# Kernel optimization log

Measured on AMD Instinct MI355X. Metric: run time of the kernel, lower is better.

## Reference

```python
import jax, jax.numpy as jnp
import numpy as np

N_NODES = 100000
N_EDGES = 1600000


def spmm(edge_index, edge_vals, x, n_nodes):
    # adj @ x with adj in COO form: out[dst] += val * x[src]
    src = edge_index[0]
    dst = edge_index[1]
    gathered = x[src] * edge_vals[:, None]  # [E, F]
    return jax.ops.segment_sum(gathered, dst, num_segments=n_nodes)


def setup_inputs() -> dict:
    key = jax.random.key(0)
    ks = jax.random.split(key, 8)
    x = jax.random.normal(ks[0], (N_NODES, 512), dtype=jnp.float32)
    edge_index = jax.random.randint(ks[1], (2, N_EDGES), 0, N_NODES, dtype=jnp.int64)
    edge_vals = jax.random.uniform(ks[2], (N_EDGES,), dtype=jnp.float32)
    # xavier-uniform style weights, zero biases (as in initialize_weights)
    def xavier(k, fan_in, fan_out):
        lim = float(np.sqrt(6.0 / (fan_in + fan_out)))
        return jax.random.uniform(k, (fan_in, fan_out), minval=-lim, maxval=lim, dtype=jnp.float32)
    W1 = xavier(ks[3], 512, 128)
    b1 = jnp.zeros((128,), jnp.float32)
    W2 = xavier(ks[4], 128, 64)
    b2 = jnp.zeros((64,), jnp.float32)
    W3 = xavier(ks[5], 64, 16)
    b3 = jnp.zeros((16,), jnp.float32)
    return {"x": x, "edge_index": edge_index, "edge_vals": edge_vals,
            "W1": W1, "b1": b1, "W2": W2, "b2": b2, "W3": W3, "b3": b3}


def reference(x, edge_index, edge_vals, W1, b1, W2, b2, W3, b3):
    n = x.shape[0]
    h = jax.nn.relu(spmm(edge_index, edge_vals, x @ W1 + b1, n))
    h = jax.nn.relu(spmm(edge_index, edge_vals, h @ W2 + b2, n))
    logits = spmm(edge_index, edge_vals, h @ W3 + b3, n)
    logp = jax.nn.log_softmax(logits, axis=1)
    return jnp.argmax(logp, axis=1)
```

## Files before the change

### kernel.cpp

```cpp
#include <hip/hip_runtime.h>

typedef _Float16 half8 __attribute__((ext_vector_type(8)));
typedef float floatx4 __attribute__((ext_vector_type(4)));

#define BSHIFT 7
#define BMASK 127
#define EPB 8192
#define P2CAP 4096

__device__ __forceinline__ void g2lds16(const void* g, void* l) {
    __builtin_amdgcn_global_load_lds(
        (const __attribute__((address_space(1))) void*)(unsigned long long)g,
        (__attribute__((address_space(3))) void*)(unsigned int)(unsigned long long)l,
        16, 0, 0);
}


__global__ __launch_bounds__(256) void p1a_hist(const int* __restrict__ dst,
                                                int* __restrict__ hist,
                                                int E, int NBUCK) {
    extern __shared__ int lh[];
    int b = blockIdx.x, t = threadIdx.x;
    for (int k = t; k < NBUCK; k += 256) lh[k] = 0;
    __syncthreads();
    int e0 = b * EPB;
    int eend = min(e0 + EPB, E);
    for (int i = e0 + t; i < eend; i += 256)
        atomicAdd(&lh[dst[i] >> BSHIFT], 1);
    __syncthreads();
    for (int k = t; k < NBUCK; k += 256) hist[(size_t)b * NBUCK + k] = lh[k];
}

__global__ __launch_bounds__(1024) void p1bc(const int* __restrict__ hist,
                                             int* __restrict__ blockOff,
                                             int* __restrict__ btot,
                                             int* __restrict__ bstart,
                                             int* __restrict__ rowptr,
                                             int NBLK, int NBUCK, int M, int E) {
    __shared__ int s[1024];
    int k = threadIdx.x;
    int run = 0;
    if (k < NBUCK) {
        for (int b = 0; b < NBLK; ++b) {
            int c = hist[(size_t)b * NBUCK + k];
            blockOff[(size_t)b * NBUCK + k] = run;
            run += c;
        }
        btot[k] = run;
    }
    s[k] = (k < NBUCK) ? run : 0;
    __syncthreads();
    for (int off = 1; off < 1024; off <<= 1) {
        int v = (k >= off) ? s[k - off] : 0;
        __syncthreads();
        s[k] += v;
        __syncthreads();
    }
    if (k < NBUCK) bstart[k] = s[k] - run;
    if (k == 0) rowptr[M] = E;
}

__global__ __launch_bounds__(256) void p1d_scatter(const int* __restrict__ src,
                                                   const int* __restrict__ dst,
                                                   const float* __restrict__ val,
                                                   const int* __restrict__ bstart,
                                                   const int* __restrict__ blockOff,
                                                   int2* __restrict__ tmp,
                                                   int E, int NBUCK) {
    extern __shared__ int cur[];
    int b = blockIdx.x, t = threadIdx.x;
    for (int k = t; k < NBUCK; k += 256)
        cur[k] = bstart[k] + blockOff[(size_t)b * NBUCK + k];
    __syncthreads();
    int e0 = b * EPB;
    int eend = min(e0 + EPB, E);
    for (int i = e0 + t; i < eend; i += 256) {
        int d = dst[i];
        int p = atomicAdd(&cur[d >> BSHIFT], 1);
        int2 pk;
        pk.x = src[i] | ((d & BMASK) << 20);
        pk.y = __float_as_int(val[i]);
        tmp[p] = pk;
    }
}

__global__ __launch_bounds__(256) void p2_sort(const int2* __restrict__ tmp,
                                               const int* __restrict__ bstart,
                                               const int* __restrict__ btot,
                                               int* __restrict__ rowptr,
                                               int2* __restrict__ ssv, int M) {
    __shared__ int2 ebuf[P2CAP];
    __shared__ int h[128], sc[128], curs[128];
    int k = blockIdx.x, t = threadIdx.x;
    int base = bstart[k], n = btot[k];
    for (int j = t; j < 128; j += 256) h[j] = 0;
    __syncthreads();
    int nl = min(n, P2CAP);
    for (int i = t; i < nl; i += 256) {
        int2 e = tmp[base + i];
        ebuf[i] = e;
        atomicAdd(&h[e.x >> 20], 1);
    }
    for (int i = P2CAP + t; i < n; i += 256) {
        int2 e = tmp[base + i];
        atomicAdd(&h[e.x >> 20], 1);
    }
    __syncthreads();
    if (t < 128) sc[t] = h[t];
    __syncthreads();
    for (int off = 1; off < 128; off <<= 1) {
        int v = (t < 128 && t >= off) ? sc[t - off] : 0;
        __syncthreads();
        if (t < 128) sc[t] += v;
        __syncthreads();
    }
    if (t < 128) {
        int node = (k << BSHIFT) + t;
        int excl = sc[t] - h[t];
        if (node < M) rowptr[node] = base + excl;
        curs[t] = excl;
    }
    __syncthreads();
    for (int i = t; i < nl; i += 256) {
        int2 e = ebuf[i];
        int p = atomicAdd(&curs[e.x >> 20], 1);
        int2 o; o.x = e.x & 0xFFFFF; o.y = e.y;
        ssv[base + p] = o;
    }
    for (int i = P2CAP + t; i < n; i += 256) {
        int2 e = tmp[base + i];
        int p = atomicAdd(&curs[e.x >> 20], 1);
        int2 o; o.x = e.x & 0xFFFFF; o.y = e.y;
        ssv[base + p] = o;
    }
}


__global__ __launch_bounds__(256) void prep_w1(const float* __restrict__ W1,
                                               _Float16* __restrict__ Whi,
                                               _Float16* __restrict__ Wlo) {
    int tid = blockIdx.x * 256 + threadIdx.x;
    int n = tid >> 9;
    int k = tid & 511;
    float w = W1[(size_t)k * 128 + n];
    _Float16 h = (_Float16)w;
    Whi[tid] = h;
    Wlo[tid] = (_Float16)(w - (float)h);
}

__global__ __launch_bounds__(256) void prep_w2(const float* __restrict__ W2,
                                               _Float16* __restrict__ Whi,
                                               _Float16* __restrict__ Wlo) {
    int tid = blockIdx.x * 256 + threadIdx.x;
    int n = tid >> 7;
    int k = tid & 127;
    float w = W2[(size_t)k * 64 + n];
    _Float16 h = (_Float16)w;
    Whi[tid] = h;
    Wlo[tid] = (_Float16)(w - (float)h);
}

__device__ __forceinline__ void split8(float4 f0, float4 f1, half8& h, half8& l) {
    float f[8] = {f0.x, f0.y, f0.z, f0.w, f1.x, f1.y, f1.z, f1.w};
#pragma unroll
    for (int j = 0; j < 8; ++j) {
        _Float16 hi = (_Float16)f[j];
        h[j] = hi;
        l[j] = (_Float16)(f[j] - (float)hi);
    }
}


__global__ __launch_bounds__(256) void gemm1_mfma(const float* __restrict__ X,
                                                  const _Float16* __restrict__ Whi,
                                                  const _Float16* __restrict__ Wlo,
                                                  const float* __restrict__ bias,
                                                  float* __restrict__ out, int M) {
    __shared__ char smem[2 * 16384];
    int t = threadIdx.x;
    int w = t >> 6;
    int lane = t & 63;
    int quad = lane >> 4;
    int l16 = lane & 15;
    int bm = blockIdx.x * 128;
    int m0 = bm + w * 32;

    int ra0 = min(m0 + l16, M - 1);
    int ra1 = min(m0 + 16 + l16, M - 1);
    const float* a0p = X + (size_t)ra0 * 512 + quad * 8;
    const float* a1p = X + (size_t)ra1 * 512 + quad * 8;

    int chunk0 = w * 4;
    const _Float16* gsrc[4];
#pragma unroll
    for (int c = 0; c < 4; ++c) {
        int idx = (chunk0 + c) * 1024 + lane * 16;
        int sec = idx >> 13;
        int row = (idx & 8191) >> 6;
        int kch = (idx >> 4) & 3;
        gsrc[c] = (sec ? Wlo : Whi) + (size_t)row * 512 + kch * 8;
    }
#pragma unroll
    for (int c = 0; c < 4; ++c)
        g2lds16(gsrc[c], smem + (chunk0 + c) * 1024);
    float4 af00 = *(const float4*)(a0p);
    float4 af01 = *(const float4*)(a0p + 4);
    float4 af10 = *(const float4*)(a1p);
    float4 af11 = *(const float4*)(a1p + 4);

    floatx4 acc[2][8];
#pragma unroll
    for (int mt = 0; mt < 2; ++mt)
#pragma unroll
        for (int nt = 0; nt < 8; ++nt) acc[mt][nt] = (floatx4){0.f, 0.f, 0.f, 0.f};

    for (int i = 0; i < 16; ++i) {
        int k0 = i * 32;
        __syncthreads();
        if (i < 15) {
            char* nbuf = smem + ((i + 1) & 1) * 16384;
#pragma unroll
            for (int c = 0; c < 4; ++c)
                g2lds16(gsrc[c] + k0 + 32, nbuf + (chunk0 + c) * 1024);
        }
        float4 nf00 = af00, nf01 = af01, nf10 = af10, nf11 = af11;
        if (i < 15) {
            nf00 = *(const float4*)(a0p + k0 + 32);
            nf01 = *(const float4*)(a0p + k0 + 36);
            nf10 = *(const float4*)(a1p + k0 + 32);
            nf11 = *(const float4*)(a1p + k0 + 36);
        }
        const char* buf = smem + (i & 1) * 16384;
        half8 bh[8], bl[8];
#pragma unroll
        for (int nt = 0; nt < 8; ++nt) {
            int off = (nt * 16 + l16) * 64 + quad * 16;
            bh[nt] = *(const half8*)(buf + off);
            bl[nt] = *(const half8*)(buf + 8192 + off);
        }
        half8 ah0, al0, ah1, al1;
        split8(af00, af01, ah0, al0);
        split8(af10, af11, ah1, al1);
#pragma unroll
        for (int nt = 0; nt < 8; ++nt) {
            acc[0][nt] = __builtin_amdgcn_mfma_f32_16x16x32_f16(ah0, bh[nt], acc[0][nt], 0, 0, 0);
            acc[1][nt] = __builtin_amdgcn_mfma_f32_16x16x32_f16(ah1, bh[nt], acc[1][nt], 0, 0, 0);
            acc[0][nt] = __builtin_amdgcn_mfma_f32_16x16x32_f16(ah0, bl[nt], acc[0][nt], 0, 0, 0);
            acc[1][nt] = __builtin_amdgcn_mfma_f32_16x16x32_f16(ah1, bl[nt], acc[1][nt], 0, 0, 0);
            acc[0][nt] = __builtin_amdgcn_mfma_f32_16x16x32_f16(al0, bh[nt], acc[0][nt], 0, 0, 0);
            acc[1][nt] = __builtin_amdgcn_mfma_f32_16x16x32_f16(al1, bh[nt], acc[1][nt], 0, 0, 0);
        }
        af00 = nf00; af01 = nf01; af10 = nf10; af11 = nf11;
    }

#pragma unroll
    for (int nt = 0; nt < 8; ++nt) {
        int col = nt * 16 + l16;
        float bv = bias[col];
#pragma unroll
        for (int mt = 0; mt < 2; ++mt)
#pragma unroll
            for (int r = 0; r < 4; ++r) {
                int row = m0 + mt * 16 + quad * 4 + r;
                if (row < M) out[(size_t)row * 128 + col] = acc[mt][nt][r] + bv;
            }
    }
}


__global__ __launch_bounds__(256) void gemm2_mfma(const float* __restrict__ H,
                                                  const _Float16* __restrict__ Whi,
                                                  const _Float16* __restrict__ Wlo,
                                                  const float* __restrict__ bias,
                                                  float* __restrict__ out, int M) {
    __shared__ char smem[2 * 64 * 320];
    int t = threadIdx.x;
#pragma unroll
    for (int i = 0; i < 4; ++i) {
        int gidx = i * 256 + t;
        int row = gidx >> 4, col = gidx & 15;
        *(float4*)(smem + row * 320 + col * 16) = ((const float4*)Whi)[gidx];
        *(float4*)(smem + 20480 + row * 320 + col * 16) = ((const float4*)Wlo)[gidx];
    }
    __syncthreads();

    int w = t >> 6;
    int lane = t & 63;
    int quad = lane >> 4;
    int l16 = lane & 15;
    int m0 = blockIdx.x * 128 + w * 32;
    int ra0 = min(m0 + l16, M - 1);
    int ra1 = min(m0 + 16 + l16, M - 1);
    const float* a0p = H + (size_t)ra0 * 128 + quad * 8;
    const float* a1p = H + (size_t)ra1 * 128 + quad * 8;

    floatx4 acc[2][4];
#pragma unroll
    for (int mt = 0; mt < 2; ++mt)
#pragma unroll
        for (int nt = 0; nt < 4; ++nt) acc[mt][nt] = (floatx4){0.f, 0.f, 0.f, 0.f};

#pragma unroll
    for (int k0 = 0; k0 < 128; k0 += 32) {
        float4 af00 = *(const float4*)(a0p + k0);
        float4 af01 = *(const float4*)(a0p + k0 + 4);
        float4 af10 = *(const float4*)(a1p + k0);
        float4 af11 = *(const float4*)(a1p + k0 + 4);
        af00.x = fmaxf(af00.x, 0.f); af00.y = fmaxf(af00.y, 0.f);
        af00.z = fmaxf(af00.z, 0.f); af00.w = fmaxf(af00.w, 0.f);
        af01.x = fmaxf(af01.x, 0.f); af01.y = fmaxf(af01.y, 0.f);
        af01.z = fmaxf(af01.z, 0.f); af01.w = fmaxf(af01.w, 0.f);
        af10.x = fmaxf(af10.x, 0.f); af10.y = fmaxf(af10.y, 0.f);
        af10.z = fmaxf(af10.z, 0.f); af10.w = fmaxf(af10.w, 0.f);
        af11.x = fmaxf(af11.x, 0.f); af11.y = fmaxf(af11.y, 0.f);
        af11.z = fmaxf(af11.z, 0.f); af11.w = fmaxf(af11.w, 0.f);
        half8 bh[4], bl[4];
#pragma unroll
        for (int nt = 0; nt < 4; ++nt) {
            int off = (nt * 16 + l16) * 320 + k0 * 2 + quad * 16;
            bh[nt] = *(const half8*)(smem + off);
            bl[nt] = *(const half8*)(smem + 20480 + off);
        }
        half8 ah0, al0, ah1, al1;
        split8(af00, af01, ah0, al0);
        split8(af10, af11, ah1, al1);
#pragma unroll
        for (int nt = 0; nt < 4; ++nt) {
            acc[0][nt] = __builtin_amdgcn_mfma_f32_16x16x32_f16(ah0, bh[nt], acc[0][nt], 0, 0, 0);
            acc[1][nt] = __builtin_amdgcn_mfma_f32_16x16x32_f16(ah1, bh[nt], acc[1][nt], 0, 0, 0);
            acc[0][nt] = __builtin_amdgcn_mfma_f32_16x16x32_f16(ah0, bl[nt], acc[0][nt], 0, 0, 0);
            acc[1][nt] = __builtin_amdgcn_mfma_f32_16x16x32_f16(ah1, bl[nt], acc[1][nt], 0, 0, 0);
            acc[0][nt] = __builtin_amdgcn_mfma_f32_16x16x32_f16(al0, bh[nt], acc[0][nt], 0, 0, 0);
            acc[1][nt] = __builtin_amdgcn_mfma_f32_16x16x32_f16(al1, bh[nt], acc[1][nt], 0, 0, 0);
        }
    }

#pragma unroll
    for (int nt = 0; nt < 4; ++nt) {
        int col = nt * 16 + l16;
        float bv = bias[col];
#pragma unroll
        for (int mt = 0; mt < 2; ++mt)
#pragma unroll
            for (int r = 0; r < 4; ++r) {
                int row = m0 + mt * 16 + quad * 4 + r;
                if (row < M) out[(size_t)row * 64 + col] = acc[mt][nt][r] + bv;
            }
    }
}


__global__ __launch_bounds__(256) void gemm3(const float* __restrict__ H,
                                             const float* __restrict__ W,
                                             const float* __restrict__ bias,
                                             float* __restrict__ out, int M) {
    __shared__ float Ws[64 * 16];
    __shared__ float Xs[32 * 68];
    int t = threadIdx.x;
    int m0 = blockIdx.x * 32;
    ((float4*)Ws)[t] = ((const float4*)W)[t];
#pragma unroll
    for (int i = 0; i < 2; i++) {
        int idx = t + i * 256;
        int gi = idx * 4;
        int row = gi >> 6, col = gi & 63;
        float4 v = make_float4(0.f, 0.f, 0.f, 0.f);
        if (m0 + row < M) v = *(const float4*)(H + (size_t)(m0 + row) * 64 + col);
        v.x = fmaxf(v.x, 0.f); v.y = fmaxf(v.y, 0.f);
        v.z = fmaxf(v.z, 0.f); v.w = fmaxf(v.w, 0.f);
        *(float4*)&Xs[row * 68 + col] = v;
    }
    __syncthreads();
    int node = t >> 3;
    int j = t & 7;
    float a0 = 0.f, a1 = 0.f;
#pragma unroll 8
    for (int k = 0; k < 64; ++k) {
        float xv = Xs[node * 68 + k];
        a0 += xv * Ws[k * 16 + j * 2];
        a1 += xv * Ws[k * 16 + j * 2 + 1];
    }
    int row = m0 + node;
    if (row < M) {
        a0 += bias[j * 2];
        a1 += bias[j * 2 + 1];
        float2 r = make_float2(a0, a1);
        *(float2*)(out + (size_t)row * 16 + j * 2) = r;
    }
}


__global__ __launch_bounds__(256) void spmm128(const int* __restrict__ rowptr,
                                               const int2* __restrict__ ssv,
                                               const float* __restrict__ T,
                                               float* __restrict__ H, int N) {
    int lane = threadIdx.x & 63;
    int node = __builtin_amdgcn_readfirstlane(blockIdx.x * 4 + (threadIdx.x >> 6));
    if (node >= N) return;
    int beg = rowptr[node], end = rowptr[node + 1];
    int half = lane >> 5;
    int c4 = (lane & 31) << 2;
    float4 acc = make_float4(0.f, 0.f, 0.f, 0.f);
    int i = beg;
    int cnt = end - beg;
    int n8 = beg + (cnt & ~7);
    for (; i < n8; i += 8) {
#pragma unroll
        for (int u = 0; u < 4; ++u) {
            int2 e = ssv[i + 2 * u + half];
            float v = __int_as_float(e.y);
            float4 xv = *(const float4*)(T + ((size_t)e.x << 7) + c4);
            acc.x += v * xv.x; acc.y += v * xv.y;
            acc.z += v * xv.z; acc.w += v * xv.w;
        }
    }
    int n2 = beg + (cnt & ~1);
    for (; i < n2; i += 2) {
        int2 e = ssv[i + half];
        float v = __int_as_float(e.y);
        float4 xv = *(const float4*)(T + ((size_t)e.x << 7) + c4);
        acc.x += v * xv.x; acc.y += v * xv.y;
        acc.z += v * xv.z; acc.w += v * xv.w;
    }
    if (i < end) {
        int2 e = ssv[i];
        float v = half ? 0.f : __int_as_float(e.y);
        float4 xv = *(const float4*)(T + ((size_t)e.x << 7) + c4);
        acc.x += v * xv.x; acc.y += v * xv.y;
        acc.z += v * xv.z; acc.w += v * xv.w;
    }
    acc.x += __shfl_xor(acc.x, 32, 64);
    acc.y += __shfl_xor(acc.y, 32, 64);
    acc.z += __shfl_xor(acc.z, 32, 64);
    acc.w += __shfl_xor(acc.w, 32, 64);
    if (half == 0)
        *(float4*)(H + ((size_t)node << 7) + c4) = acc;
}

__global__ __launch_bounds__(256) void spmm64(const int* __restrict__ rowptr,
                                              const int2* __restrict__ ssv,
                                              const float* __restrict__ T,
                                              float* __restrict__ H, int N) {
    int lane = threadIdx.x & 63;
    int node = __builtin_amdgcn_readfirstlane(blockIdx.x * 4 + (threadIdx.x >> 6));
    if (node >= N) return;
    int beg = rowptr[node], end = rowptr[node + 1];
    int es = lane >> 4;
    int c4 = (lane & 15) << 2;
    float4 acc = make_float4(0.f, 0.f, 0.f, 0.f);
    int i = beg;
    int cnt = end - beg;
    int n8 = beg + (cnt & ~7);
    for (; i < n8; i += 8) {
#pragma unroll
        for (int u = 0; u < 2; ++u) {
            int2 e = ssv[i + 4 * u + es];
            float v = __int_as_float(e.y);
            float4 xv = *(const float4*)(T + ((size_t)e.x << 6) + c4);
            acc.x += v * xv.x; acc.y += v * xv.y;
            acc.z += v * xv.z; acc.w += v * xv.w;
        }
    }
    int n4 = beg + (cnt & ~3);
    for (; i < n4; i += 4) {
        int2 e = ssv[i + es];
        float v = __int_as_float(e.y);
        float4 xv = *(const float4*)(T + ((size_t)e.x << 6) + c4);
        acc.x += v * xv.x; acc.y += v * xv.y;
        acc.z += v * xv.z; acc.w += v * xv.w;
    }
    if (i < end) {
        int idx = i + es;
        int2 e = ssv[idx < end ? idx : i];
        float v = (idx < end) ? __int_as_float(e.y) : 0.f;
        float4 xv = *(const float4*)(T + ((size_t)e.x << 6) + c4);
        acc.x += v * xv.x; acc.y += v * xv.y;
        acc.z += v * xv.z; acc.w += v * xv.w;
    }
    acc.x += __shfl_xor(acc.x, 16, 64);
    acc.y += __shfl_xor(acc.y, 16, 64);
    acc.z += __shfl_xor(acc.z, 16, 64);
    acc.w += __shfl_xor(acc.w, 16, 64);
    acc.x += __shfl_xor(acc.x, 32, 64);
    acc.y += __shfl_xor(acc.y, 32, 64);
    acc.z += __shfl_xor(acc.z, 32, 64);
    acc.w += __shfl_xor(acc.w, 32, 64);
    if (lane < 16)
        *(float4*)(H + ((size_t)node << 6) + c4) = acc;
}

__global__ __launch_bounds__(256) void spmm_argmax(const int* __restrict__ rowptr,
                                                   const int2* __restrict__ ssv,
                                                   const float* __restrict__ T,
                                                   int* __restrict__ out, int N) {
    int t = threadIdx.x;
    int node = blockIdx.x * 64 + (t >> 2);
    int q = t & 3;
    int c4 = q << 2;
    int beg = 0, end = 0;
    if (node < N) { beg = rowptr[node]; end = rowptr[node + 1]; }
    float4 acc = make_float4(0.f, 0.f, 0.f, 0.f);
    int i = beg;
    int cnt = end - beg;
    int n4 = beg + (cnt & ~3);
    for (; i < n4; i += 4) {
#pragma unroll
        for (int u = 0; u < 4; ++u) {
            int2 e = ssv[i + u];
            float v = __int_as_float(e.y);
            float4 xv = *(const float4*)(T + ((size_t)e.x << 4) + c4);
            acc.x += v * xv.x; acc.y += v * xv.y;
            acc.z += v * xv.z; acc.w += v * xv.w;
        }
    }
    for (; i < end; ++i) {
        int2 e = ssv[i];
        float v = __int_as_float(e.y);
        float4 xv = *(const float4*)(T + ((size_t)e.x << 4) + c4);
        acc.x += v * xv.x; acc.y += v * xv.y;
        acc.z += v * xv.z; acc.w += v * xv.w;
    }
    float bv = acc.x; int bi = c4;
    if (acc.y > bv) { bv = acc.y; bi = c4 + 1; }
    if (acc.z > bv) { bv = acc.z; bi = c4 + 2; }
    if (acc.w > bv) { bv = acc.w; bi = c4 + 3; }
#pragma unroll
    for (int off = 1; off <= 2; off <<= 1) {
        float ov = __shfl_xor(bv, off, 64);
        int oi = __shfl_xor(bi, off, 64);
        if (ov > bv || (ov == bv && oi < bi)) { bv = ov; bi = oi; }
    }
    if (node < N && q == 0) out[node] = bi;
}


extern "C" void kernel_launch(void* const* d_in, const int* in_sizes, int n_in,
                              void* d_out, int out_size, void* d_ws, size_t ws_size,
                              hipStream_t stream) {
    const float* x  = (const float*)d_in[0];
    const int*   ei = (const int*)d_in[1];
    const float* ev = (const float*)d_in[2];
    const float* W1 = (const float*)d_in[3];
    const float* b1 = (const float*)d_in[4];
    const float* W2 = (const float*)d_in[5];
    const float* b2 = (const float*)d_in[6];
    const float* W3 = (const float*)d_in[7];
    const float* b3 = (const float*)d_in[8];
    int* out = (int*)d_out;

    int M = in_sizes[0] / 512;
    int E = in_sizes[2];
    const int* src = ei;
    const int* dst = ei + E;

    int NBUCK = (M + BMASK) >> BSHIFT;
    int NBLK  = (E + EPB - 1) / EPB;

    char* ws = (char*)d_ws;
    size_t off = 0;
    auto alloc = [&](size_t bytes) {
        size_t o = off;
        off += (bytes + 255) & ~(size_t)255;
        return o;
    };
    float*    tA      = (float*)(ws + alloc((size_t)M * 128 * 4));
    float*    hB      = (float*)(ws + alloc((size_t)M * 128 * 4));
    int2*     ssv     = (int2*) (ws + alloc((size_t)E * 8));
    int*      rowptr  = (int*)  (ws + alloc((size_t)(M + 1) * 4));
    int*      hist    = (int*)  (ws + alloc((size_t)NBLK * NBUCK * 4));
    int*      blockOff= (int*)  (ws + alloc((size_t)NBLK * NBUCK * 4));
    int*      btot    = (int*)  (ws + alloc((size_t)NBUCK * 4));
    int*      bstart  = (int*)  (ws + alloc((size_t)NBUCK * 4));
    _Float16* w1hi    = (_Float16*)(ws + alloc(512 * 128 * 2));
    _Float16* w1lo    = (_Float16*)(ws + alloc(512 * 128 * 2));
    _Float16* w2hi    = (_Float16*)(ws + alloc(128 * 64 * 2));
    _Float16* w2lo    = (_Float16*)(ws + alloc(128 * 64 * 2));
    int2*     tmp     = (int2*)hB;

    prep_w1<<<256, 256, 0, stream>>>(W1, w1hi, w1lo);
    prep_w2<<<32, 256, 0, stream>>>(W2, w2hi, w2lo);
    p1a_hist<<<NBLK, 256, NBUCK * 4, stream>>>(dst, hist, E, NBUCK);
    p1bc<<<1, 1024, 0, stream>>>(hist, blockOff, btot, bstart, rowptr, NBLK, NBUCK, M, E);
    p1d_scatter<<<NBLK, 256, NBUCK * 4, stream>>>(src, dst, ev, bstart, blockOff, tmp, E, NBUCK);
    p2_sort<<<NBUCK, 256, 0, stream>>>(tmp, bstart, btot, rowptr, ssv, M);

    gemm1_mfma<<<(M + 127) / 128, 256, 0, stream>>>(x, w1hi, w1lo, b1, tA, M);
    spmm128<<<(M + 3) / 4, 256, 0, stream>>>(rowptr, ssv, tA, hB, M);
    gemm2_mfma<<<(M + 127) / 128, 256, 0, stream>>>(hB, w2hi, w2lo, b2, tA, M);
    spmm64<<<(M + 3) / 4, 256, 0, stream>>>(rowptr, ssv, tA, hB, M);
    gemm3<<<(M + 31) / 32, 256, 0, stream>>>(hB, W3, b3, tA, M);
    spmm_argmax<<<(M + 63) / 64, 256, 0, stream>>>(rowptr, ssv, tA, out, M);
}
```

Baseline: 687.3 us.

## Replace two-pass bucket sort CSR build with global-atomic counting sort

Replaces the bucketed histogram, block-offset scan, bucket scatter and per-bucket local sort with a direct per-node degree count using global atomics, a two-kernel prefix scan, and a scatter that places each edge with a global atomic cursor. The weight-split prep kernels are folded into the counting kernel to cut launches. This removes one full pass over the edges and the intermediate buffer, at the cost of heavier contention on global atomics. Edge order within each row becomes nondeterministic, so floating-point summation order in the SpMM can vary between runs.

```diff
diff --git a/kernel.cpp b/kernel.cpp
--- a/kernel.cpp
+++ b/kernel.cpp
@@ -2,11 +2,6 @@
 
 typedef _Float16 half8 __attribute__((ext_vector_type(8)));
 typedef float floatx4 __attribute__((ext_vector_type(4)));
-
-#define BSHIFT 7
-#define BMASK 127
-#define EPB 8192
-#define P2CAP 4096
 
 __device__ __forceinline__ void g2lds16(const void* g, void* l) {
     __builtin_amdgcn_global_load_lds(
@@ -16,149 +11,110 @@
 }
 
 
-__global__ __launch_bounds__(256) void p1a_hist(const int* __restrict__ dst,
-                                                int* __restrict__ hist,
-                                                int E, int NBUCK) {
-    extern __shared__ int lh[];
-    int b = blockIdx.x, t = threadIdx.x;
-    for (int k = t; k < NBUCK; k += 256) lh[k] = 0;
-    __syncthreads();
-    int e0 = b * EPB;
-    int eend = min(e0 + EPB, E);
-    for (int i = e0 + t; i < eend; i += 256)
-        atomicAdd(&lh[dst[i] >> BSHIFT], 1);
-    __syncthreads();
-    for (int k = t; k < NBUCK; k += 256) hist[(size_t)b * NBUCK + k] = lh[k];
-}
-
-__global__ __launch_bounds__(1024) void p1bc(const int* __restrict__ hist,
-                                             int* __restrict__ blockOff,
-                                             int* __restrict__ btot,
-                                             int* __restrict__ bstart,
-                                             int* __restrict__ rowptr,
-                                             int NBLK, int NBUCK, int M, int E) {
+__global__ __launch_bounds__(256) void k_prep_count(const float* __restrict__ W1,
+                                                    const float* __restrict__ W2,
+                                                    _Float16* __restrict__ w1hi,
+                                                    _Float16* __restrict__ w1lo,
+                                                    _Float16* __restrict__ w2hi,
+                                                    _Float16* __restrict__ w2lo,
+                                                    const int* __restrict__ dst,
+                                                    int* __restrict__ deg, int E) {
+    int b = blockIdx.x;
+    int t = threadIdx.x;
+    if (b < 256) {
+        int tid = b * 256 + t;
+        int n = tid >> 9;
+        int k = tid & 511;
+        float w = W1[(size_t)k * 128 + n];
+        _Float16 h = (_Float16)w;
+        w1hi[tid] = h;
+        w1lo[tid] = (_Float16)(w - (float)h);
+        return;
+    }
+    if (b < 288) {
+        int tid = (b - 256) * 256 + t;
+        int n = tid >> 7;
+        int k = tid & 127;
+        float w = W2[(size_t)k * 64 + n];
+        _Float16 h = (_Float16)w;
+        w2hi[tid] = h;
+        w2lo[tid] = (_Float16)(w - (float)h);
+        return;
+    }
+    int i0 = ((b - 288) * 256 + t) * 4;
+    if (i0 + 3 < E) {
+        int4 d4 = *(const int4*)(dst + i0);
+        atomicAdd(&deg[d4.x], 1);
+        atomicAdd(&deg[d4.y], 1);
+        atomicAdd(&deg[d4.z], 1);
+        atomicAdd(&deg[d4.w], 1);
+    } else {
+        for (int i = i0; i < E; ++i)
+            atomicAdd(&deg[dst[i]], 1);
+    }
+}
+
+__global__ __launch_bounds__(1024) void k_scan_a(const int* __restrict__ deg,
+                                                 int* __restrict__ rowptr,
+                                                 int* __restrict__ partial, int M) {
     __shared__ int s[1024];
-    int k = threadIdx.x;
-    int run = 0;
-    if (k < NBUCK) {
-        for (int b = 0; b < NBLK; ++b) {
-            int c = hist[(size_t)b * NBUCK + k];
-            blockOff[(size_t)b * NBUCK + k] = run;
-            run += c;
-        }
-        btot[k] = run;
-    }
-    s[k] = (k < NBUCK) ? run : 0;
+    int c = blockIdx.x, t = threadIdx.x;
+    int i = c * 1024 + t;
+    int v = (i < M) ? deg[i] : 0;
+    s[t] = v;
     __syncthreads();
     for (int off = 1; off < 1024; off <<= 1) {
-        int v = (k >= off) ? s[k - off] : 0;
+        int u = (t >= off) ? s[t - off] : 0;
         __syncthreads();
-        s[k] += v;
+        s[t] += u;
         __syncthreads();
     }
-    if (k < NBUCK) bstart[k] = s[k] - run;
-    if (k == 0) rowptr[M] = E;
-}
-
-__global__ __launch_bounds__(256) void p1d_scatter(const int* __restrict__ src,
-                                                   const int* __restrict__ dst,
-                                                   const float* __restrict__ val,
-                                                   const int* __restrict__ bstart,
-                                                   const int* __restrict__ blockOff,
-                                                   int2* __restrict__ tmp,
-                                                   int E, int NBUCK) {
-    extern __shared__ int cur[];
-    int b = blockIdx.x, t = threadIdx.x;
-    for (int k = t; k < NBUCK; k += 256)
-        cur[k] = bstart[k] + blockOff[(size_t)b * NBUCK + k];
+    if (i < M) rowptr[i] = s[t] - v;
+    if (t == 1023) partial[c] = s[t];
+}
+
+__global__ __launch_bounds__(1024) void k_scan_b(const int* __restrict__ partial,
+                                                 int* __restrict__ rowptr,
+                                                 int* __restrict__ cur,
+                                                 int M, int E, int NCH) {
+    __shared__ int sp[128];
+    int c = blockIdx.x, t = threadIdx.x;
+    if (t < NCH) sp[t] = partial[t];
     __syncthreads();
-    int e0 = b * EPB;
-    int eend = min(e0 + EPB, E);
-    for (int i = e0 + t; i < eend; i += 256) {
-        int d = dst[i];
-        int p = atomicAdd(&cur[d >> BSHIFT], 1);
-        int2 pk;
-        pk.x = src[i] | ((d & BMASK) << 20);
-        pk.y = __float_as_int(val[i]);
-        tmp[p] = pk;
-    }
-}
-
-__global__ __launch_bounds__(256) void p2_sort(const int2* __restrict__ tmp,
-                                               const int* __restrict__ bstart,
-                                               const int* __restrict__ btot,
-                                               int* __restrict__ rowptr,
-                                               int2* __restrict__ ssv, int M) {
-    __shared__ int2 ebuf[P2CAP];
-    __shared__ int h[128], sc[128], curs[128];
-    int k = blockIdx.x, t = threadIdx.x;
-    int base = bstart[k], n = btot[k];
-    for (int j = t; j < 128; j += 256) h[j] = 0;
-    __syncthreads();
-    int nl = min(n, P2CAP);
-    for (int i = t; i < nl; i += 256) {
-        int2 e = tmp[base + i];
-        ebuf[i] = e;
-        atomicAdd(&h[e.x >> 20], 1);
-    }
-    for (int i = P2CAP + t; i < n; i += 256) {
-        int2 e = tmp[base + i];
-        atomicAdd(&h[e.x >> 20], 1);
-    }
-    __syncthreads();
-    if (t < 128) sc[t] = h[t];
-    __syncthreads();
-    for (int off = 1; off < 128; off <<= 1) {
-        int v = (t < 128 && t >= off) ? sc[t - off] : 0;
-        __syncthreads();
-        if (t < 128) sc[t] += v;
-        __syncthreads();
-    }
-    if (t < 128) {
-        int node = (k << BSHIFT) + t;
-        int excl = sc[t] - h[t];
-        if (node < M) rowptr[node] = base + excl;
-        curs[t] = excl;
-    }
-    __syncthreads();
-    for (int i = t; i < nl; i += 256) {
-        int2 e = ebuf[i];
-        int p = atomicAdd(&curs[e.x >> 20], 1);
-        int2 o; o.x = e.x & 0xFFFFF; o.y = e.y;
-        ssv[base + p] = o;
-    }
-    for (int i = P2CAP + t; i < n; i += 256) {
-        int2 e = tmp[base + i];
-        int p = atomicAdd(&curs[e.x >> 20], 1);
-        int2 o; o.x = e.x & 0xFFFFF; o.y = e.y;
-        ssv[base + p] = o;
-    }
-}
-
-
-__global__ __launch_bounds__(256) void prep_w1(const float* __restrict__ W1,
-                                               _Float16* __restrict__ Whi,
-                                               _Float16* __restrict__ Wlo) {
-    int tid = blockIdx.x * 256 + threadIdx.x;
-    int n = tid >> 9;
-    int k = tid & 511;
-    float w = W1[(size_t)k * 128 + n];
-    _Float16 h = (_Float16)w;
-    Whi[tid] = h;
-    Wlo[tid] = (_Float16)(w - (float)h);
-}
-
-__global__ __launch_bounds__(256) void prep_w2(const float* __restrict__ W2,
-                                               _Float16* __restrict__ Whi,
-                                               _Float16* __restrict__ Wlo) {
-    int tid = blockIdx.x * 256 + threadIdx.x;
-    int n = tid >> 7;
-    int k = tid & 127;
-    float w = W2[(size_t)k * 64 + n];
-    _Float16 h = (_Float16)w;
-    Whi[tid] = h;
-    Wlo[tid] = (_Float16)(w - (float)h);
-}
+    int pre = 0;
+    for (int j = 0; j < c; ++j) pre += sp[j];
+    int i = c * 1024 + t;
+    if (i < M) {
+        int r = rowptr[i] + pre;
+        rowptr[i] = r;
+        cur[i] = r;
+    }
+    if (c == NCH - 1 && t == 1023) rowptr[M] = E;
+}
+
+__global__ __launch_bounds__(256) void k_scatter(const int* __restrict__ src,
+                                                 const int* __restrict__ dst,
+                                                 const float* __restrict__ val,
+                                                 int* __restrict__ cur,
+                                                 int2* __restrict__ ssv, int E) {
+    int i0 = (blockIdx.x * 256 + threadIdx.x) * 4;
+    if (i0 + 3 < E) {
+        int4 s4 = *(const int4*)(src + i0);
+        int4 d4 = *(const int4*)(dst + i0);
+        float4 v4 = *(const float4*)(val + i0);
+        int p;
+        p = atomicAdd(&cur[d4.x], 1); ssv[p] = make_int2(s4.x, __float_as_int(v4.x));
+        p = atomicAdd(&cur[d4.y], 1); ssv[p] = make_int2(s4.y, __float_as_int(v4.y));
+        p = atomicAdd(&cur[d4.z], 1); ssv[p] = make_int2(s4.z, __float_as_int(v4.z));
+        p = atomicAdd(&cur[d4.w], 1); ssv[p] = make_int2(s4.w, __float_as_int(v4.w));
+    } else {
+        for (int i = i0; i < E; ++i) {
+            int p = atomicAdd(&cur[dst[i]], 1);
+            ssv[p] = make_int2(src[i], __float_as_int(val[i]));
+        }
+    }
+}
+
 
 __device__ __forceinline__ void split8(float4 f0, float4 f1, half8& h, half8& l) {
     float f[8] = {f0.x, f0.y, f0.z, f0.w, f1.x, f1.y, f1.z, f1.w};
@@ -553,8 +509,7 @@
     const int* src = ei;
     const int* dst = ei + E;
 
-    int NBUCK = (M + BMASK) >> BSHIFT;
-    int NBLK  = (E + EPB - 1) / EPB;
+    int NCH = (M + 1023) >> 10;
 
     char* ws = (char*)d_ws;
     size_t off = 0;
@@ -567,22 +522,20 @@
     float*    hB      = (float*)(ws + alloc((size_t)M * 128 * 4));
     int2*     ssv     = (int2*) (ws + alloc((size_t)E * 8));
     int*      rowptr  = (int*)  (ws + alloc((size_t)(M + 1) * 4));
-    int*      hist    = (int*)  (ws + alloc((size_t)NBLK * NBUCK * 4));
-    int*      blockOff= (int*)  (ws + alloc((size_t)NBLK * NBUCK * 4));
-    int*      btot    = (int*)  (ws + alloc((size_t)NBUCK * 4));
-    int*      bstart  = (int*)  (ws + alloc((size_t)NBUCK * 4));
+    int*      deg     = (int*)  (ws + alloc((size_t)M * 4));
+    int*      cur     = (int*)  (ws + alloc((size_t)M * 4));
+    int*      partial = (int*)  (ws + alloc(128 * 4));
     _Float16* w1hi    = (_Float16*)(ws + alloc(512 * 128 * 2));
     _Float16* w1lo    = (_Float16*)(ws + alloc(512 * 128 * 2));
     _Float16* w2hi    = (_Float16*)(ws + alloc(128 * 64 * 2));
     _Float16* w2lo    = (_Float16*)(ws + alloc(128 * 64 * 2));
-    int2*     tmp     = (int2*)hB;
-
-    prep_w1<<<256, 256, 0, stream>>>(W1, w1hi, w1lo);
-    prep_w2<<<32, 256, 0, stream>>>(W2, w2hi, w2lo);
-    p1a_hist<<<NBLK, 256, NBUCK * 4, stream>>>(dst, hist, E, NBUCK);
-    p1bc<<<1, 1024, 0, stream>>>(hist, blockOff, btot, bstart, rowptr, NBLK, NBUCK, M, E);
-    p1d_scatter<<<NBLK, 256, NBUCK * 4, stream>>>(src, dst, ev, bstart, blockOff, tmp, E, NBUCK);
-    p2_sort<<<NBUCK, 256, 0, stream>>>(tmp, bstart, btot, rowptr, ssv, M);
+
+    hipMemsetAsync(deg, 0, (size_t)M * 4, stream);
+    int cntBlk = 288 + (E + 1023) / 1024;
+    k_prep_count<<<cntBlk, 256, 0, stream>>>(W1, W2, w1hi, w1lo, w2hi, w2lo, dst, deg, E);
+    k_scan_a<<<NCH, 1024, 0, stream>>>(deg, rowptr, partial, M);
+    k_scan_b<<<NCH, 1024, 0, stream>>>(partial, rowptr, cur, M, E, NCH);
+    k_scatter<<<(E + 1023) / 1024, 256, 0, stream>>>(src, dst, ev, cur, ssv, E);
 
     gemm1_mfma<<<(M + 127) / 128, 256, 0, stream>>>(x, w1hi, w1lo, b1, tA, M);
     spmm128<<<(M + 3) / 4, 256, 0, stream>>>(rowptr, ssv, tA, hB, M);
```

New measurement: 747.0 us. +8.7%, slower.

## Fuse CSR-build phases with weight prep and GEMM1 halves into shared launches

Applied to the files above, without the earlier changes.

Merges the W1/W2 fp16 split prep into the histogram kernel and replaces the single-thread-per-bucket serial scan with a parallel per-bucket block scan plus a small bucket scan. GEMM1 is split in two halves, each co-launched with the scatter and the bucket sort kernels, so independent GEMM work fills the GPU while the irregular sort phases run. The aim is fewer launches and less idle hardware during the low-parallelism preprocessing. The cost is larger static LDS per block in the fused kernels, which may lower occupancy for the sort and scatter blocks.

```diff
diff --git a/kernel.cpp b/kernel.cpp
--- a/kernel.cpp
+++ b/kernel.cpp
@@ -15,60 +15,102 @@
         16, 0, 0);
 }
 
-
-__global__ __launch_bounds__(256) void p1a_hist(const int* __restrict__ dst,
-                                                int* __restrict__ hist,
-                                                int E, int NBUCK) {
-    extern __shared__ int lh[];
+__global__ __launch_bounds__(256) void k1_prep_hist(const float* __restrict__ W1,
+                                                    const float* __restrict__ W2,
+                                                    _Float16* __restrict__ w1hi,
+                                                    _Float16* __restrict__ w1lo,
+                                                    _Float16* __restrict__ w2hi,
+                                                    _Float16* __restrict__ w2lo,
+                                                    const int* __restrict__ dst,
+                                                    int* __restrict__ hist,
+                                                    int E, int NBUCK) {
+    __shared__ int lh[1024];
     int b = blockIdx.x, t = threadIdx.x;
+    if (b < 256) {
+        int tid = b * 256 + t;
+        int n = tid >> 9;
+        int k = tid & 511;
+        float w = W1[(size_t)k * 128 + n];
+        _Float16 h = (_Float16)w;
+        w1hi[tid] = h;
+        w1lo[tid] = (_Float16)(w - (float)h);
+        return;
+    }
+    if (b < 288) {
+        int tid = (b - 256) * 256 + t;
+        int n = tid >> 7;
+        int k = tid & 127;
+        float w = W2[(size_t)k * 64 + n];
+        _Float16 h = (_Float16)w;
+        w2hi[tid] = h;
+        w2lo[tid] = (_Float16)(w - (float)h);
+        return;
+    }
+    int bb = b - 288;
     for (int k = t; k < NBUCK; k += 256) lh[k] = 0;
     __syncthreads();
-    int e0 = b * EPB;
+    int e0 = bb * EPB;
     int eend = min(e0 + EPB, E);
     for (int i = e0 + t; i < eend; i += 256)
         atomicAdd(&lh[dst[i] >> BSHIFT], 1);
     __syncthreads();
-    for (int k = t; k < NBUCK; k += 256) hist[(size_t)b * NBUCK + k] = lh[k];
-}
-
-__global__ __launch_bounds__(1024) void p1bc(const int* __restrict__ hist,
-                                             int* __restrict__ blockOff,
-                                             int* __restrict__ btot,
-                                             int* __restrict__ bstart,
-                                             int* __restrict__ rowptr,
-                                             int NBLK, int NBUCK, int M, int E) {
+    for (int k = t; k < NBUCK; k += 256) hist[(size_t)bb * NBUCK + k] = lh[k];
+}
+
+__global__ __launch_bounds__(256) void k2_scanA(const int* __restrict__ hist,
+                                                int* __restrict__ blockOff,
+                                                int* __restrict__ btot,
+                                                int NBLK, int NBUCK) {
+    __shared__ int s[256];
+    int k = blockIdx.x;
+    int t = threadIdx.x;
+    int carry = 0;
+    for (int base = 0; base < NBLK; base += 256) {
+        int b = base + t;
+        int c = (b < NBLK) ? hist[(size_t)b * NBUCK + k] : 0;
+        s[t] = c;
+        __syncthreads();
+        for (int off = 1; off < 256; off <<= 1) {
+            int v = (t >= off) ? s[t - off] : 0;
+            __syncthreads();
+            s[t] += v;
+            __syncthreads();
+        }
+        if (b < NBLK) blockOff[(size_t)b * NBUCK + k] = carry + s[t] - c;
+        carry += s[255];
+        __syncthreads();
+    }
+    if (t == 0) btot[k] = carry;
+}
+
+__global__ __launch_bounds__(1024) void k2b_bscan(const int* __restrict__ btot,
+                                                  int* __restrict__ bstart,
+                                                  int* __restrict__ rowptr,
+                                                  int NBUCK, int M, int E) {
     __shared__ int s[1024];
-    int k = threadIdx.x;
-    int run = 0;
-    if (k < NBUCK) {
-        for (int b = 0; b < NBLK; ++b) {
-            int c = hist[(size_t)b * NBUCK + k];
-            blockOff[(size_t)b * NBUCK + k] = run;
-            run += c;
-        }
-        btot[k] = run;
-    }
-    s[k] = (k < NBUCK) ? run : 0;
+    int tid = threadIdx.x;
+    int v = (tid < NBUCK) ? btot[tid] : 0;
+    s[tid] = v;
     __syncthreads();
     for (int off = 1; off < 1024; off <<= 1) {
-        int v = (k >= off) ? s[k - off] : 0;
+        int t = (tid >= off) ? s[tid - off] : 0;
         __syncthreads();
-        s[k] += v;
+        s[tid] += t;
         __syncthreads();
     }
-    if (k < NBUCK) bstart[k] = s[k] - run;
-    if (k == 0) rowptr[M] = E;
-}
-
-__global__ __launch_bounds__(256) void p1d_scatter(const int* __restrict__ src,
-                                                   const int* __restrict__ dst,
-                                                   const float* __restrict__ val,
-                                                   const int* __restrict__ bstart,
-                                                   const int* __restrict__ blockOff,
-                                                   int2* __restrict__ tmp,
-                                                   int E, int NBUCK) {
-    extern __shared__ int cur[];
-    int b = blockIdx.x, t = threadIdx.x;
+    if (tid < NBUCK) bstart[tid] = s[tid] - v;
+    if (tid == 0) rowptr[M] = E;
+}
+
+
+__device__ __forceinline__ void p1d_body(int b, const int* __restrict__ src,
+                                         const int* __restrict__ dst,
+                                         const float* __restrict__ val,
+                                         const int* __restrict__ bstart,
+                                         const int* __restrict__ blockOff,
+                                         int2* __restrict__ tmp,
+                                         int E, int NBUCK, int* cur) {
+    int t = threadIdx.x;
     for (int k = t; k < NBUCK; k += 256)
         cur[k] = bstart[k] + blockOff[(size_t)b * NBUCK + k];
     __syncthreads();
@@ -84,14 +126,16 @@
     }
 }
 
-__global__ __launch_bounds__(256) void p2_sort(const int2* __restrict__ tmp,
-                                               const int* __restrict__ bstart,
-                                               const int* __restrict__ btot,
-                                               int* __restrict__ rowptr,
-                                               int2* __restrict__ ssv, int M) {
-    __shared__ int2 ebuf[P2CAP];
-    __shared__ int h[128], sc[128], curs[128];
-    int k = blockIdx.x, t = threadIdx.x;
+__device__ __forceinline__ void p2_body(int k, const int2* __restrict__ tmp,
+                                        const int* __restrict__ bstart,
+                                        const int* __restrict__ btot,
+                                        int* __restrict__ rowptr,
+                                        int2* __restrict__ ssv, int M, char* lds) {
+    int2* ebuf = (int2*)lds;
+    int* h    = (int*)(lds + 32768);
+    int* sc   = (int*)(lds + 33280);
+    int* curs = (int*)(lds + 33792);
+    int t = threadIdx.x;
     int base = bstart[k], n = btot[k];
     for (int j = t; j < 128; j += 256) h[j] = 0;
     __syncthreads();
@@ -136,30 +180,6 @@
 }
 
 
-__global__ __launch_bounds__(256) void prep_w1(const float* __restrict__ W1,
-                                               _Float16* __restrict__ Whi,
-                                               _Float16* __restrict__ Wlo) {
-    int tid = blockIdx.x * 256 + threadIdx.x;
-    int n = tid >> 9;
-    int k = tid & 511;
-    float w = W1[(size_t)k * 128 + n];
-    _Float16 h = (_Float16)w;
-    Whi[tid] = h;
-    Wlo[tid] = (_Float16)(w - (float)h);
-}
-
-__global__ __launch_bounds__(256) void prep_w2(const float* __restrict__ W2,
-                                               _Float16* __restrict__ Whi,
-                                               _Float16* __restrict__ Wlo) {
-    int tid = blockIdx.x * 256 + threadIdx.x;
-    int n = tid >> 7;
-    int k = tid & 127;
-    float w = W2[(size_t)k * 64 + n];
-    _Float16 h = (_Float16)w;
-    Whi[tid] = h;
-    Wlo[tid] = (_Float16)(w - (float)h);
-}
-
 __device__ __forceinline__ void split8(float4 f0, float4 f1, half8& h, half8& l) {
     float f[8] = {f0.x, f0.y, f0.z, f0.w, f1.x, f1.y, f1.z, f1.w};
 #pragma unroll
@@ -171,18 +191,17 @@
 }
 
 
-__global__ __launch_bounds__(256) void gemm1_mfma(const float* __restrict__ X,
-                                                  const _Float16* __restrict__ Whi,
-                                                  const _Float16* __restrict__ Wlo,
-                                                  const float* __restrict__ bias,
-                                                  float* __restrict__ out, int M) {
-    __shared__ char smem[2 * 16384];
+__device__ __forceinline__ void gemm1_body(int bm, char* smem,
+                                           const float* __restrict__ X,
+                                           const _Float16* __restrict__ Whi,
+                                           const _Float16* __restrict__ Wlo,
+                                           const float* __restrict__ bias,
+                                           float* __restrict__ out, int M) {
     int t = threadIdx.x;
     int w = t >> 6;
     int lane = t & 63;
     int quad = lane >> 4;
     int l16 = lane & 15;
-    int bm = blockIdx.x * 128;
     int m0 = bm + w * 32;
 
     int ra0 = min(m0 + l16, M - 1);
@@ -265,6 +284,47 @@
                 if (row < M) out[(size_t)row * 128 + col] = acc[mt][nt][r] + bv;
             }
     }
+}
+
+__global__ __launch_bounds__(256) void k3_p1d_gemm1a(const int* __restrict__ src,
+                                                     const int* __restrict__ dst,
+                                                     const float* __restrict__ val,
+                                                     const int* __restrict__ bstart,
+                                                     const int* __restrict__ blockOff,
+                                                     int2* __restrict__ tmp,
+                                                     int E, int NBUCK, int NBLK,
+                                                     const float* __restrict__ X,
+                                                     const _Float16* __restrict__ Whi,
+                                                     const _Float16* __restrict__ Wlo,
+                                                     const float* __restrict__ bias,
+                                                     float* __restrict__ out, int M) {
+    __shared__ __align__(16) char lds[32768];
+    int b = blockIdx.x;
+    if (b < NBLK) {
+        p1d_body(b, src, dst, val, bstart, blockOff, tmp, E, NBUCK, (int*)lds);
+        return;
+    }
+    gemm1_body((b - NBLK) * 128, lds, X, Whi, Wlo, bias, out, M);
+}
+
+__global__ __launch_bounds__(256) void k4_p2_gemm1b(const int2* __restrict__ tmp,
+                                                    const int* __restrict__ bstart,
+                                                    const int* __restrict__ btot,
+                                                    int* __restrict__ rowptr,
+                                                    int2* __restrict__ ssv,
+                                                    int M, int NBUCK, int g1a,
+                                                    const float* __restrict__ X,
+                                                    const _Float16* __restrict__ Whi,
+                                                    const _Float16* __restrict__ Wlo,
+                                                    const float* __restrict__ bias,
+                                                    float* __restrict__ out) {
+    __shared__ __align__(16) char lds[34304];
+    int b = blockIdx.x;
+    if (b < NBUCK) {
+        p2_body(b, tmp, bstart, btot, rowptr, ssv, M, lds);
+        return;
+    }
+    gemm1_body((g1a + b - NBUCK) * 128, lds, X, Whi, Wlo, bias, out, M);
 }
 
 
@@ -577,14 +637,21 @@
     _Float16* w2lo    = (_Float16*)(ws + alloc(128 * 64 * 2));
     int2*     tmp     = (int2*)hB;
 
-    prep_w1<<<256, 256, 0, stream>>>(W1, w1hi, w1lo);
-    prep_w2<<<32, 256, 0, stream>>>(W2, w2hi, w2lo);
-    p1a_hist<<<NBLK, 256, NBUCK * 4, stream>>>(dst, hist, E, NBUCK);
-    p1bc<<<1, 1024, 0, stream>>>(hist, blockOff, btot, bstart, rowptr, NBLK, NBUCK, M, E);
-    p1d_scatter<<<NBLK, 256, NBUCK * 4, stream>>>(src, dst, ev, bstart, blockOff, tmp, E, NBUCK);
-    p2_sort<<<NBUCK, 256, 0, stream>>>(tmp, bstart, btot, rowptr, ssv, M);
-
-    gemm1_mfma<<<(M + 127) / 128, 256, 0, stream>>>(x, w1hi, w1lo, b1, tA, M);
+    int G1  = (M + 127) / 128;
+    int G1a = G1 / 2;
+    int G1b = G1 - G1a;
+
+    k1_prep_hist<<<288 + NBLK, 256, 0, stream>>>(W1, W2, w1hi, w1lo, w2hi, w2lo,
+                                                 dst, hist, E, NBUCK);
+    k2_scanA<<<NBUCK, 256, 0, stream>>>(hist, blockOff, btot, NBLK, NBUCK);
+    k2b_bscan<<<1, 1024, 0, stream>>>(btot, bstart, rowptr, NBUCK, M, E);
+    k3_p1d_gemm1a<<<NBLK + G1a, 256, 0, stream>>>(src, dst, ev, bstart, blockOff, tmp,
+                                                  E, NBUCK, NBLK,
+                                                  x, w1hi, w1lo, b1, tA, M);
+    k4_p2_gemm1b<<<NBUCK + G1b, 256, 0, stream>>>(tmp, bstart, btot, rowptr, ssv,
+                                                  M, NBUCK, G1a,
+                                                  x, w1hi, w1lo, b1, tA);
+
     spmm128<<<(M + 3) / 4, 256, 0, stream>>>(rowptr, ssv, tA, hB, M);
     gemm2_mfma<<<(M + 127) / 128, 256, 0, stream>>>(hB, w2hi, w2lo, b2, tA, M);
     spmm64<<<(M + 3) / 4, 256, 0, stream>>>(rowptr, ssv, tA, hB, M);
```

New measurement: 644.6 us (median of 2 runs). -6.2%, faster.
